# Performance work log

Hardware: AMD Instinct MI355X
Metric: run time of the kernel (lower is better)

## Reference

```python
import jax, jax.numpy as jnp
import numpy as np

B, T, D, H = 16, 81, 128, 8  # batch, ntok, d_model (= d_head), n_head


def setup_inputs() -> dict:
    key = jax.random.key(0)
    ks = jax.random.split(key, 6)
    s = 0.02
    return {
        "x": jax.random.normal(ks[0], (B, T, D), jnp.float32),
        "msk": jnp.ones((1, H, T, T), jnp.float32),
        "wqkv_w": jax.random.normal(ks[1], (H * 2 * D, D), jnp.float32) * s,
        "wqkv_b": jax.random.normal(ks[2], (H * 2 * D,), jnp.float32) * s,
        "wk_w": jax.random.normal(ks[3], (H, D), jnp.float32) * s,
        "fanout_w": jax.random.normal(ks[4], (D, D), jnp.float32) * s,
        "fanout_b": jax.random.normal(ks[5], (D,), jnp.float32) * s,
        "head_enabled": jnp.ones((H,), jnp.float32),
        "n": 0, "layer": 0, "pas": 1,
    }


def quick_gelu(x):
    return x * jax.nn.sigmoid(1.702 * x)


def reference(x, msk, wqkv_w, wqkv_b, wk_w, fanout_w, fanout_b, head_enabled, n, layer, pas):
    b, t, d = x.shape
    h = wk_w.shape[0]
    # qkv projection: per-head q and v of full width d (d_head == d_model)
    y = x @ wqkv_w.T + wqkv_b                      # [b, t, h*2*d]
    y = y.reshape(b, t, h, 2 * d)
    q, v = y[..., :d], y[..., d:]                  # [b, t, h, d] each
    # k: input gated per-head by wk.weight rows
    k = x[:, :, None, :] * wk_w[None, None, :, :]  # [b, t, h, d]
    # v gating by head-enabled flags
    v = v * head_enabled[None, None, :, None]
    # L1 attention scores: a[b,h,t,s] = -sum_d |q[b,t,h,d] - k[b,s,h,d]| / sqrt(d)
    diff = jnp.abs(q[:, :, None, :, :] - k[:, None, :, :, :])  # [b, t, s, h, d]
    a = -diff.sum(-1)                               # [b, t, s, h]
    a = jnp.transpose(a, (0, 3, 1, 2)) / jnp.sqrt(jnp.asarray(d, x.dtype))  # [b,h,t,s]
    a = jax.nn.softmax(a, axis=3) * msk
    bo = jnp.einsum('bhts,bshd->bthd', a, v)        # [b, t, h, d]
    bo = bo.sum(axis=2)                             # sum over heads -> [b, t, d]
    ap = jnp.transpose(a[0] - 1.0 + msk[0], (1, 2, 0))  # [t, s, h]
    z = quick_gelu(bo + 4.0) - 4.0
    z = z @ fanout_w.T + fanout_b
    return (x + z, ap)
```

## Files before the change

### kernel.cpp

```cpp
#include <hip/hip_runtime.h>
#include <math.h>

#define Bq 16
#define Tq 81
#define Dq 128
#define Hq 8
#define BT (Bq*Tq)
#define BTD (Bq*Tq*Dq)
#define PS 84
#define P_SZ   (Bq*Tq*Hq*PS)
#define QV_SZ  (BT*Hq*Dq)
#define P_OFF  0
#define Q_OFF  (P_OFF + P_SZ)
#define V_OFF  (Q_OFF + QV_SZ)
#define XB_OFF (V_OFF + QV_SZ)
#define XB_FSZ (BTD/2)
#define WB_OFF (XB_OFF + XB_FSZ)

typedef __attribute__((ext_vector_type(8))) short short8;
typedef __attribute__((ext_vector_type(4))) float f32x4;

__device__ __forceinline__ float l1_4(const float4 q, const float4 k) {
    return fabsf(q.x - k.x) + fabsf(q.y - k.y) + fabsf(q.z - k.z) + fabsf(q.w - k.w);
}
__device__ __forceinline__ int imin(int a, int b) { return a < b ? a : b; }
__device__ __forceinline__ unsigned short f2bf(float f) {
    unsigned u = __float_as_uint(f);
    u += 0x7fffu + ((u >> 16) & 1u);
    return (unsigned short)(u >> 16);
}

__global__ __launch_bounds__(256) void k_prep(
    const float* __restrict__ w, const float* __restrict__ x,
    unsigned short* __restrict__ Wb, unsigned short* __restrict__ xb)
{
    const int NW4 = (Hq * 2 * Dq * Dq) / 4;
    const int NX4 = BTD / 4;
    const int idx = blockIdx.x * 256 + threadIdx.x;
    if (idx < NW4) {
        const float4 v = ((const float4*)w)[idx];
        ushort4 o;
        o.x = f2bf(v.x); o.y = f2bf(v.y); o.z = f2bf(v.z); o.w = f2bf(v.w);
        ((ushort4*)Wb)[idx] = o;
    } else if (idx < NW4 + NX4) {
        const int j = idx - NW4;
        const float4 v = ((const float4*)x)[j];
        ushort4 o;
        o.x = f2bf(v.x); o.y = f2bf(v.y); o.z = f2bf(v.z); o.w = f2bf(v.w);
        ((ushort4*)xb)[j] = o;
    }
}

__global__ __launch_bounds__(256) void k_qkv_mfma(
    const unsigned short* __restrict__ xb, const unsigned short* __restrict__ Wb,
    const float* __restrict__ bias, const float* __restrict__ he,
    float* __restrict__ Qo, float* __restrict__ Vo)
{
    const int tid = threadIdx.x;
    const int w = tid >> 6, lane = tid & 63;
    const int ln = lane & 15, quad = lane >> 4;
    const int mt = blockIdx.x * 4 + w;
    const int n0 = blockIdx.y * 64;
    const int h  = blockIdx.y >> 2;
    const int isV = (blockIdx.y >> 1) & 1;
    const int c0 = (blockIdx.y & 1) * 64;

    const int row = mt * 16 + ln;
    const int arow = row < BT ? row : BT - 1;
    const unsigned short* xa  = xb + (size_t)arow * Dq + quad * 8;
    const unsigned short* wb0 = Wb + (size_t)(n0 + ln) * Dq + quad * 8;

    f32x4 acc[4];
    #pragma unroll
    for (int i = 0; i < 4; ++i) acc[i] = (f32x4){0.f, 0.f, 0.f, 0.f};

    #pragma unroll
    for (int kb = 0; kb < Dq; kb += 32) {
        const short8 af = *(const short8*)(xa + kb);
        #pragma unroll
        for (int nt = 0; nt < 4; ++nt) {
            const short8 bf = *(const short8*)(wb0 + (size_t)(nt * 16) * Dq + kb);
            acc[nt] = __builtin_amdgcn_mfma_f32_16x16x32_bf16(af, bf, acc[nt], 0, 0, 0);
        }
    }

    if (mt >= 81) return;
    const float scale = isV ? he[h] : 1.0f;
    float* dst = isV ? Vo : Qo;
    const int gm0 = mt * 16 + quad * 4;
    #pragma unroll
    for (int nt = 0; nt < 4; ++nt) {
        const float bn = bias[n0 + nt * 16 + ln];
        #pragma unroll
        for (int r = 0; r < 4; ++r) {
            const int gm = gm0 + r;
            dst[((size_t)gm * Hq + h) * Dq + c0 + nt * 16 + ln] =
                (acc[nt][r] + bn) * scale;
        }
    }
}

__global__ __launch_bounds__(256) void k_scores(
    const float* __restrict__ x, const float* __restrict__ Q,
    const float* __restrict__ wk, const float* __restrict__ msk,
    float* __restrict__ P)
{
    __shared__ float Kl[81 * 132];
    __shared__ float sc[21 * 85];
    __shared__ float rsum[24];
    const int tid = threadIdx.x;
    const int tq = blockIdx.x, h = blockIdx.y, b = blockIdx.z;
    const int t0g = tq * 21;
    const int nt = (tq == 3) ? 18 : 21;

    {
        const float* wkb = wk + (size_t)h * Dq;
        for (int idx = tid; idx < Tq * 32; idx += 256) {
            const int r = idx >> 5, c = idx & 31;
            const float4 xv = *(const float4*)(x + (size_t)(b * Tq + r) * Dq + c * 4);
            const float4 wv = *(const float4*)(wkb + c * 4);
            float4 kv;
            kv.x = xv.x * wv.x; kv.y = xv.y * wv.y;
            kv.z = xv.z * wv.z; kv.w = xv.w * wv.w;
            *(float4*)(&Kl[r * 132 + c * 4]) = kv;
        }
    }
    __syncthreads();

    if (tid < 252) {
        const int tg = tid / 12, sg = tid % 12;
        const int t = imin(t0g + tg, Tq - 1);
        const float* qrow = Q + ((size_t)(b * Tq + t) * Hq + h) * Dq;

        int sidx[7];
        #pragma unroll
        for (int j = 0; j < 7; ++j) sidx[j] = imin(sg + 12 * j, Tq - 1);

        float acc[7];
        #pragma unroll
        for (int j = 0; j < 7; ++j) acc[j] = 0.f;

        #pragma unroll 4
        for (int k4 = 0; k4 < 32; ++k4) {
            const float4 qv = *(const float4*)(qrow + k4 * 4);
            #pragma unroll
            for (int j = 0; j < 7; ++j) {
                const float4 kv = *(const float4*)(&Kl[sidx[j] * 132 + k4 * 4]);
                acc[j] += l1_4(qv, kv);
            }
        }
        const float ns = -0.08838834764831845f;
        #pragma unroll
        for (int j = 0; j < 7; ++j)
            sc[tg * 85 + sg + 12 * j] = acc[j] * ns;
    }
    __syncthreads();

    {
        const int w = tid >> 6, lane = tid & 63;
        for (int r = w; r < nt; r += 4) {
            float* row = sc + r * 85;
            const bool hi = (lane + 64) < Tq;
            const float v0 = row[lane];
            const float v1 = hi ? row[lane + 64] : -1e30f;
            float m = fmaxf(v0, v1);
            #pragma unroll
            for (int off = 32; off > 0; off >>= 1)
                m = fmaxf(m, __shfl_xor(m, off));
            const float e0 = __expf(v0 - m);
            const float e1 = hi ? __expf(v1 - m) : 0.f;
            float s = e0 + e1;
            #pragma unroll
            for (int off = 32; off > 0; off >>= 1)
                s += __shfl_xor(s, off);
            row[lane] = e0;
            if (hi) row[lane + 64] = e1;
            if (lane == 0) rsum[r] = 1.0f / s;
        }
    }
    __syncthreads();

    for (int idx = tid; idx < nt * Tq; idx += 256) {
        const int tl = idx / Tq, s = idx - tl * Tq;
        const int tg2 = t0g + tl;
        const float mv = msk[((size_t)h * Tq + tg2) * Tq + s];
        const float pm = sc[tl * 85 + s] * rsum[tl] * mv;
        P[(((size_t)b * Tq + tg2) * Hq + h) * PS + s] = pm;
    }
}

__global__ __launch_bounds__(256) void k_ap(
    const float* __restrict__ P, const float* __restrict__ msk,
    float* __restrict__ out)
{
    const int t = blockIdx.x;
    const float* Pt = P + ((size_t)t * Hq) * PS;
    float* apb = out + BTD + (size_t)t * Tq * Hq;
    for (int idx = threadIdx.x; idx < Tq * Hq; idx += 256) {
        const int h = idx & 7, s = idx >> 3;
        const float mv = msk[((size_t)h * Tq + t) * Tq + s];
        apb[(size_t)s * Hq + h] = Pt[(size_t)h * PS + s] - 1.0f + mv;
    }
}

__global__ __launch_bounds__(256) void k_out(
    const float* __restrict__ x, const float* __restrict__ P,
    const float* __restrict__ V, const float* __restrict__ fw,
    const float* __restrict__ fb, float* __restrict__ out)
{
    __shared__ float Pl[4][Hq][PS];
    __shared__ float bo_part[4][4][128];
    __shared__ float zs[4][128];
    const int tid = threadIdx.x;
    const int t0 = blockIdx.x * 4, b = blockIdx.y;

    {
        const float4* src = (const float4*)(P + ((size_t)b * Tq + t0) * Hq * PS);
        #pragma unroll
        for (int idx = tid; idx < 4 * Hq * PS / 4; idx += 256)
            ((float4*)Pl)[idx] = src[idx];
    }
    __syncthreads();

    const int w = tid >> 6, lane = tid & 63;
    {
        const int d0 = lane * 2;
        const int h0 = w * 2, h1 = h0 + 1;
        float2 acc[4];
        #pragma unroll
        for (int i = 0; i < 4; ++i) acc[i] = make_float2(0.f, 0.f);
        const float* v0p = V + ((size_t)(b * Tq) * Hq + h0) * Dq + d0;
        const float* v1p = V + ((size_t)(b * Tq) * Hq + h1) * Dq + d0;
        for (int s4 = 0; s4 < 20; ++s4) {
            float4 p0[4], p1[4];
            #pragma unroll
            for (int t = 0; t < 4; ++t) {
                p0[t] = *(const float4*)(&Pl[t][h0][s4 * 4]);
                p1[t] = *(const float4*)(&Pl[t][h1][s4 * 4]);
            }
            #pragma unroll
            for (int ss = 0; ss < 4; ++ss) {
                const int s = s4 * 4 + ss;
                const float2 v0 = *(const float2*)(v0p + (size_t)s * Hq * Dq);
                const float2 v1 = *(const float2*)(v1p + (size_t)s * Hq * Dq);
                #pragma unroll
                for (int t = 0; t < 4; ++t) {
                    const float a0 = ((const float*)&p0[t])[ss];
                    const float a1 = ((const float*)&p1[t])[ss];
                    acc[t].x += a0 * v0.x + a1 * v1.x;
                    acc[t].y += a0 * v0.y + a1 * v1.y;
                }
            }
        }
        {
            const float2 v0 = *(const float2*)(v0p + (size_t)80 * Hq * Dq);
            const float2 v1 = *(const float2*)(v1p + (size_t)80 * Hq * Dq);
            #pragma unroll
            for (int t = 0; t < 4; ++t) {
                const float a0 = Pl[t][h0][80], a1 = Pl[t][h1][80];
                acc[t].x += a0 * v0.x + a1 * v1.x;
                acc[t].y += a0 * v0.y + a1 * v1.y;
            }
        }
        #pragma unroll
        for (int t = 0; t < 4; ++t) {
            bo_part[w][t][d0]     = acc[t].x;
            bo_part[w][t][d0 + 1] = acc[t].y;
        }
    }
    __syncthreads();

    #pragma unroll
    for (int idx = tid; idx < 512; idx += 256) {
        const int t = idx >> 7, d = idx & 127;
        const float bo = bo_part[0][t][d] + bo_part[1][t][d]
                       + bo_part[2][t][d] + bo_part[3][t][d];
        const float tt = bo + 4.0f;
        const float sg = 1.0f / (1.0f + __expf(-1.702f * tt));
        zs[t][d] = tt * sg - 4.0f;
    }
    __syncthreads();

    {
        const int n = tid & 127;
        const float* fwr = fw + (size_t)n * Dq;
        const float fbn = fb[n];
        #pragma unroll
        for (int i = 0; i < 2; ++i) {
            const int t = (tid >> 7) + 2 * i;
            float a = 0.f;
            #pragma unroll 8
            for (int k4 = 0; k4 < 32; ++k4) {
                const float4 z4 = *(const float4*)(&zs[t][k4 * 4]);
                const float4 w4 = *(const float4*)(fwr + k4 * 4);
                a += z4.x * w4.x + z4.y * w4.y + z4.z * w4.z + z4.w * w4.w;
            }
            const int tg2 = t0 + t;
            if (tg2 < Tq) {
                const size_t o = ((size_t)b * Tq + tg2) * Dq + n;
                out[o] = x[o] + a + fbn;
            }
        }
    }
}

extern "C" void kernel_launch(void* const* d_in, const int* in_sizes, int n_in,
                              void* d_out, int out_size, void* d_ws, size_t ws_size,
                              hipStream_t stream) {
    const float* x        = (const float*)d_in[0];
    const float* msk      = (const float*)d_in[1];
    const float* wqkv_w   = (const float*)d_in[2];
    const float* wqkv_b   = (const float*)d_in[3];
    const float* wk_w     = (const float*)d_in[4];
    const float* fanout_w = (const float*)d_in[5];
    const float* fanout_b = (const float*)d_in[6];
    const float* he       = (const float*)d_in[7];
    float* out = (float*)d_out;
    float* ws  = (float*)d_ws;

    float* P   = ws + P_OFF;
    float* Q   = ws + Q_OFF;
    float* V   = ws + V_OFF;
    unsigned short* xb = (unsigned short*)(ws + XB_OFF);
    unsigned short* Wb = (unsigned short*)(ws + WB_OFF);

    k_prep<<<dim3(418), 256, 0, stream>>>(wqkv_w, x, Wb, xb);
    k_qkv_mfma<<<dim3(21, 32), 256, 0, stream>>>(xb, Wb, wqkv_b, he, Q, V);
    k_scores<<<dim3(4, 8, 16), 256, 0, stream>>>(x, Q, wk_w, msk, P);
    k_ap<<<dim3(81), 256, 0, stream>>>(P, msk, out);
    k_out<<<dim3(21, 16), 256, 0, stream>>>(x, P, V, fanout_w, fanout_b, out);
}
```

Baseline: 138.5 us.

## Relayout Q/V head-major, register-block L1 scores, fuse ap output, widen output blocks

The QKV kernel now writes Q and V in [b,h,t,d] order, so later kernels read contiguous per-head rows. The score kernel register-blocks 3 queries by 4 keys per thread, so each K tile loaded from shared memory is reused across queries; it uses fewer active threads (147 of 256) to do this. The separate ap kernel is removed: batch-0 blocks of the score kernel write the ap output directly, saving one launch and one re-read of P. The output kernel now handles 8 tokens per 512-thread block with one head per wave, which reuses each V load across more tokens and cuts the block count. The last block in the final batch reads past the end of P into the neighbouring workspace; those rows are never written out.

```diff
diff --git a/kernel.cpp b/kernel.cpp
--- a/kernel.cpp
+++ b/kernel.cpp
@@ -94,7 +94,8 @@
         #pragma unroll
         for (int r = 0; r < 4; ++r) {
             const int gm = gm0 + r;
-            dst[((size_t)gm * Hq + h) * Dq + c0 + nt * 16 + ln] =
+            const int bb = gm / 81, tt = gm - bb * 81;
+            dst[(((size_t)bb * Hq + h) * Tq + tt) * Dq + c0 + nt * 16 + ln] =
                 (acc[nt][r] + bn) * scale;
         }
     }
@@ -103,7 +104,7 @@
 __global__ __launch_bounds__(256) void k_scores(
     const float* __restrict__ x, const float* __restrict__ Q,
     const float* __restrict__ wk, const float* __restrict__ msk,
-    float* __restrict__ P)
+    float* __restrict__ P, float* __restrict__ out)
 {
     __shared__ float Kl[81 * 132];
     __shared__ float sc[21 * 85];
@@ -127,32 +128,46 @@
     }
     __syncthreads();
 
-    if (tid < 252) {
-        const int tg = tid / 12, sg = tid % 12;
-        const int t = imin(t0g + tg, Tq - 1);
-        const float* qrow = Q + ((size_t)(b * Tq + t) * Hq + h) * Dq;
-
-        int sidx[7];
-        #pragma unroll
-        for (int j = 0; j < 7; ++j) sidx[j] = imin(sg + 12 * j, Tq - 1);
-
-        float acc[7];
-        #pragma unroll
-        for (int j = 0; j < 7; ++j) acc[j] = 0.f;
-
-        #pragma unroll 4
+    if (tid < 147) {
+        const int tg = tid / 21, sg = tid % 21;
+        const float* qrow[3];
+        #pragma unroll
+        for (int i = 0; i < 3; ++i) {
+            const int t = imin(t0g + tg * 3 + i, Tq - 1);
+            qrow[i] = Q + (((size_t)b * Hq + h) * Tq + t) * Dq;
+        }
+        int sidx[4];
+        #pragma unroll
+        for (int j = 0; j < 4; ++j) sidx[j] = imin(sg + 21 * j, Tq - 1);
+
+        float acc[3][4];
+        #pragma unroll
+        for (int i = 0; i < 3; ++i)
+            #pragma unroll
+            for (int j = 0; j < 4; ++j) acc[i][j] = 0.f;
+
+        #pragma unroll 2
         for (int k4 = 0; k4 < 32; ++k4) {
-            const float4 qv = *(const float4*)(qrow + k4 * 4);
-            #pragma unroll
-            for (int j = 0; j < 7; ++j) {
-                const float4 kv = *(const float4*)(&Kl[sidx[j] * 132 + k4 * 4]);
-                acc[j] += l1_4(qv, kv);
+            float4 kv[4];
+            #pragma unroll
+            for (int j = 0; j < 4; ++j)
+                kv[j] = *(const float4*)(&Kl[sidx[j] * 132 + k4 * 4]);
+            #pragma unroll
+            for (int i = 0; i < 3; ++i) {
+                const float4 qv = *(const float4*)(qrow[i] + k4 * 4);
+                #pragma unroll
+                for (int j = 0; j < 4; ++j)
+                    acc[i][j] += l1_4(qv, kv[j]);
             }
         }
         const float ns = -0.08838834764831845f;
         #pragma unroll
-        for (int j = 0; j < 7; ++j)
-            sc[tg * 85 + sg + 12 * j] = acc[j] * ns;
+        for (int i = 0; i < 3; ++i) {
+            const int tl = tg * 3 + i;
+            #pragma unroll
+            for (int j = 0; j < 4; ++j)
+                sc[tl * 85 + sg + 21 * j] = acc[i][j] * ns;
+        }
     }
     __syncthreads();
 
@@ -180,44 +195,32 @@
     }
     __syncthreads();
 
+    const bool doap = (b == 0);
     for (int idx = tid; idx < nt * Tq; idx += 256) {
         const int tl = idx / Tq, s = idx - tl * Tq;
         const int tg2 = t0g + tl;
         const float mv = msk[((size_t)h * Tq + tg2) * Tq + s];
         const float pm = sc[tl * 85 + s] * rsum[tl] * mv;
         P[(((size_t)b * Tq + tg2) * Hq + h) * PS + s] = pm;
-    }
-}
-
-__global__ __launch_bounds__(256) void k_ap(
-    const float* __restrict__ P, const float* __restrict__ msk,
-    float* __restrict__ out)
-{
-    const int t = blockIdx.x;
-    const float* Pt = P + ((size_t)t * Hq) * PS;
-    float* apb = out + BTD + (size_t)t * Tq * Hq;
-    for (int idx = threadIdx.x; idx < Tq * Hq; idx += 256) {
-        const int h = idx & 7, s = idx >> 3;
-        const float mv = msk[((size_t)h * Tq + t) * Tq + s];
-        apb[(size_t)s * Hq + h] = Pt[(size_t)h * PS + s] - 1.0f + mv;
-    }
-}
-
-__global__ __launch_bounds__(256) void k_out(
+        if (doap) out[BTD + ((size_t)tg2 * Tq + s) * Hq + h] = pm - 1.0f + mv;
+    }
+}
+
+__global__ __launch_bounds__(512) void k_out(
     const float* __restrict__ x, const float* __restrict__ P,
     const float* __restrict__ V, const float* __restrict__ fw,
     const float* __restrict__ fb, float* __restrict__ out)
 {
-    __shared__ float Pl[4][Hq][PS];
-    __shared__ float bo_part[4][4][128];
-    __shared__ float zs[4][128];
+    __shared__ float Pl[8][Hq][PS];
+    __shared__ float bo_part[8][8][128];
+    __shared__ float zs[8][128];
     const int tid = threadIdx.x;
-    const int t0 = blockIdx.x * 4, b = blockIdx.y;
+    const int t0 = blockIdx.x * 8, b = blockIdx.y;
 
     {
         const float4* src = (const float4*)(P + ((size_t)b * Tq + t0) * Hq * PS);
         #pragma unroll
-        for (int idx = tid; idx < 4 * Hq * PS / 4; idx += 256)
+        for (int idx = tid; idx < 8 * Hq * PS / 4; idx += 512)
             ((float4*)Pl)[idx] = src[idx];
     }
     __syncthreads();
@@ -225,45 +228,38 @@
     const int w = tid >> 6, lane = tid & 63;
     {
         const int d0 = lane * 2;
-        const int h0 = w * 2, h1 = h0 + 1;
-        float2 acc[4];
-        #pragma unroll
-        for (int i = 0; i < 4; ++i) acc[i] = make_float2(0.f, 0.f);
-        const float* v0p = V + ((size_t)(b * Tq) * Hq + h0) * Dq + d0;
-        const float* v1p = V + ((size_t)(b * Tq) * Hq + h1) * Dq + d0;
+        float2 acc[8];
+        #pragma unroll
+        for (int i = 0; i < 8; ++i) acc[i] = make_float2(0.f, 0.f);
+        const float* vp = V + (((size_t)b * Hq + w) * Tq) * Dq + d0;
         for (int s4 = 0; s4 < 20; ++s4) {
-            float4 p0[4], p1[4];
-            #pragma unroll
-            for (int t = 0; t < 4; ++t) {
-                p0[t] = *(const float4*)(&Pl[t][h0][s4 * 4]);
-                p1[t] = *(const float4*)(&Pl[t][h1][s4 * 4]);
-            }
+            float4 p[8];
+            #pragma unroll
+            for (int t = 0; t < 8; ++t)
+                p[t] = *(const float4*)(&Pl[t][w][s4 * 4]);
             #pragma unroll
             for (int ss = 0; ss < 4; ++ss) {
                 const int s = s4 * 4 + ss;
-                const float2 v0 = *(const float2*)(v0p + (size_t)s * Hq * Dq);
-                const float2 v1 = *(const float2*)(v1p + (size_t)s * Hq * Dq);
+                const float2 vv = *(const float2*)(vp + (size_t)s * Dq);
                 #pragma unroll
-                for (int t = 0; t < 4; ++t) {
-                    const float a0 = ((const float*)&p0[t])[ss];
-                    const float a1 = ((const float*)&p1[t])[ss];
-                    acc[t].x += a0 * v0.x + a1 * v1.x;
-                    acc[t].y += a0 * v0.y + a1 * v1.y;
+                for (int t = 0; t < 8; ++t) {
+                    const float pv = ((const float*)&p[t])[ss];
+                    acc[t].x = fmaf(pv, vv.x, acc[t].x);
+                    acc[t].y = fmaf(pv, vv.y, acc[t].y);
                 }
             }
         }
         {
-            const float2 v0 = *(const float2*)(v0p + (size_t)80 * Hq * Dq);
-            const float2 v1 = *(const float2*)(v1p + (size_t)80 * Hq * Dq);
-            #pragma unroll
-            for (int t = 0; t < 4; ++t) {
-                const float a0 = Pl[t][h0][80], a1 = Pl[t][h1][80];
-                acc[t].x += a0 * v0.x + a1 * v1.x;
-                acc[t].y += a0 * v0.y + a1 * v1.y;
+            const float2 vv = *(const float2*)(vp + (size_t)80 * Dq);
+            #pragma unroll
+            for (int t = 0; t < 8; ++t) {
+                const float pv = Pl[t][w][80];
+                acc[t].x = fmaf(pv, vv.x, acc[t].x);
+                acc[t].y = fmaf(pv, vv.y, acc[t].y);
             }
         }
         #pragma unroll
-        for (int t = 0; t < 4; ++t) {
+        for (int t = 0; t < 8; ++t) {
             bo_part[w][t][d0]     = acc[t].x;
             bo_part[w][t][d0 + 1] = acc[t].y;
         }
@@ -271,10 +267,11 @@
     __syncthreads();
 
     #pragma unroll
-    for (int idx = tid; idx < 512; idx += 256) {
+    for (int idx = tid; idx < 1024; idx += 512) {
         const int t = idx >> 7, d = idx & 127;
-        const float bo = bo_part[0][t][d] + bo_part[1][t][d]
-                       + bo_part[2][t][d] + bo_part[3][t][d];
+        float bo = 0.f;
+        #pragma unroll
+        for (int ww = 0; ww < 8; ++ww) bo += bo_part[ww][t][d];
         const float tt = bo + 4.0f;
         const float sg = 1.0f / (1.0f + __expf(-1.702f * tt));
         zs[t][d] = tt * sg - 4.0f;
@@ -282,24 +279,26 @@
     __syncthreads();
 
     {
-        const int n = tid & 127;
+        const int n = tid & 127, tg = tid >> 7;
         const float* fwr = fw + (size_t)n * Dq;
         const float fbn = fb[n];
-        #pragma unroll
-        for (int i = 0; i < 2; ++i) {
-            const int t = (tid >> 7) + 2 * i;
-            float a = 0.f;
-            #pragma unroll 8
-            for (int k4 = 0; k4 < 32; ++k4) {
-                const float4 z4 = *(const float4*)(&zs[t][k4 * 4]);
-                const float4 w4 = *(const float4*)(fwr + k4 * 4);
-                a += z4.x * w4.x + z4.y * w4.y + z4.z * w4.z + z4.w * w4.w;
-            }
-            const int tg2 = t0 + t;
-            if (tg2 < Tq) {
-                const size_t o = ((size_t)b * Tq + tg2) * Dq + n;
-                out[o] = x[o] + a + fbn;
-            }
+        float a0 = 0.f, a1 = 0.f;
+        #pragma unroll 8
+        for (int k4 = 0; k4 < 32; ++k4) {
+            const float4 w4 = *(const float4*)(fwr + k4 * 4);
+            const float4 z0 = *(const float4*)(&zs[tg][k4 * 4]);
+            const float4 z1 = *(const float4*)(&zs[tg + 4][k4 * 4]);
+            a0 += z0.x * w4.x + z0.y * w4.y + z0.z * w4.z + z0.w * w4.w;
+            a1 += z1.x * w4.x + z1.y * w4.y + z1.z * w4.z + z1.w * w4.w;
+        }
+        const int t1 = t0 + tg, t2 = t0 + tg + 4;
+        if (t1 < Tq) {
+            const size_t o = ((size_t)b * Tq + t1) * Dq + n;
+            out[o] = x[o] + a0 + fbn;
+        }
+        if (t2 < Tq) {
+            const size_t o = ((size_t)b * Tq + t2) * Dq + n;
+            out[o] = x[o] + a1 + fbn;
         }
     }
 }
@@ -326,7 +325,6 @@
 
     k_prep<<<dim3(418), 256, 0, stream>>>(wqkv_w, x, Wb, xb);
     k_qkv_mfma<<<dim3(21, 32), 256, 0, stream>>>(xb, Wb, wqkv_b, he, Q, V);
-    k_scores<<<dim3(4, 8, 16), 256, 0, stream>>>(x, Q, wk_w, msk, P);
-    k_ap<<<dim3(81), 256, 0, stream>>>(P, msk, out);
-    k_out<<<dim3(21, 16), 256, 0, stream>>>(x, P, V, fanout_w, fanout_b, out);
-}
+    k_scores<<<dim3(4, 8, 16), 256, 0, stream>>>(x, Q, wk_w, msk, P, out);
+    k_out<<<dim3(11, 16), 512, 0, stream>>>(x, P, V, fanout_w, fanout_b, out);
+}
```

Measured after the change: 130.7 us. -5.6%, faster.
